# Kernel tuning notes

Hardware: AMD Instinct MI355X
Metric: run time of the kernel (lower is better)

## Reference

```python
import jax, jax.numpy as jnp
import numpy as np

FF = 256      # ff_dim
LAT = 128     # latent_dim
ACT = 8       # action_dim
VIS = 512     # vis_dim
MIN_VAR = 0.01


def _lin(x, w, b):
    return x @ w.T + b


def _mlp2(x, w1, b1, w2, b2):
    return jax.nn.relu(_lin(jax.nn.relu(_lin(x, w1, b1)), w2, b2))


def setup_inputs() -> dict:
    key = jax.random.key(0)
    ks = jax.random.split(key, 20)
    def W(k, o, i):
        return jax.random.normal(k, (o, i), jnp.float32) / np.sqrt(i).astype(np.float32)
    def Bv(o):
        return jnp.zeros((o,), jnp.float32)
    B, T = 512, 128
    return {
        'vis_feats': jax.random.normal(ks[0], (B, T, VIS), jnp.float32),
        'actions':   jax.random.normal(ks[1], (B, T - 1, ACT), jnp.float32),
        'noise':     jax.random.normal(ks[2], (T, B, LAT), jnp.float32),
        # _obs_encode
        'w_obs1': W(ks[3], FF, VIS), 'b_obs1': Bv(FF),
        'w_obs2': W(ks[4], FF, FF),  'b_obs2': Bv(FF),
        # _gru_in
        'w_gin': W(ks[5], FF, LAT + ACT), 'b_gin': Bv(FF),
        # GRU (single layer, input FF, hidden FF)
        'w_ih': W(ks[6], 3 * FF, FF), 'w_hh': W(ks[7], 3 * FF, FF),
        'b_ih': Bv(3 * FF), 'b_hh': Bv(3 * FF),
        # _prior_layers / heads
        'w_pr1': W(ks[8], FF, FF),  'b_pr1': Bv(FF),
        'w_pr2': W(ks[9], FF, FF),  'b_pr2': Bv(FF),
        'w_prm': W(ks[10], LAT, FF), 'b_prm': Bv(LAT),
        'w_prv': W(ks[11], LAT, FF), 'b_prv': Bv(LAT),
        # _post_layers / heads (input is concat(belief, obs) -> 2*FF)
        'w_po1': W(ks[12], FF, 2 * FF), 'b_po1': Bv(FF),
        'w_po2': W(ks[13], FF, FF),     'b_po2': Bv(FF),
        'w_pom': W(ks[14], LAT, FF), 'b_pom': Bv(LAT),
        'w_pov': W(ks[15], LAT, FF), 'b_pov': Bv(LAT),
    }


def _forward(vis_feats, actions, noise,
             w_obs1, b_obs1, w_obs2, b_obs2,
             w_gin, b_gin, w_ih, w_hh, b_ih, b_hh,
             w_pr1, b_pr1, w_pr2, b_pr2, w_prm, b_prm, w_prv, b_prv,
             w_po1, b_po1, w_po2, b_po2, w_pom, b_pom, w_pov, b_pov):
    # encode: obs MLP over precomputed visual features -> [B,T,FF]
    obs = _mlp2(vis_feats, w_obs1, b_obs1, w_obs2, b_obs2)
    B = obs.shape[0]

    def posterior(belief, o, eps):
        mid = _mlp2(jnp.concatenate([belief, o], -1), w_po1, b_po1, w_po2, b_po2)
        mu = _lin(mid, w_pom, b_pom)
        var = jnp.exp(_lin(mid, w_pov, b_pov)) + MIN_VAR  # diag covariance
        return mu + jnp.sqrt(var) * eps, mu, var          # rsample

    # initial posterior with zero rnn belief
    s0, _, _ = posterior(jnp.zeros((B, FF), obs.dtype), obs[:, 0], noise[0])
    h0 = jnp.zeros((B, FF), obs.dtype)

    xs = (jnp.swapaxes(actions, 0, 1),          # [T-1,B,ACT]
          jnp.swapaxes(obs[:, 1:], 0, 1),       # [T-1,B,FF]
          noise[1:])                             # [T-1,B,LAT]

    def step(carry, x):
        s, h = carry
        a, o, eps = x
        g = jax.nn.relu(_lin(jnp.concatenate([s, a], -1), w_gin, b_gin))
        # GRU cell (PyTorch gate layout: r,z,n)
        gi = _lin(g, w_ih, b_ih)
        gh = _lin(h, w_hh, b_hh)
        ir, iz, inn = jnp.split(gi, 3, -1)
        hr, hz, hn = jnp.split(gh, 3, -1)
        r = jax.nn.sigmoid(ir + hr)
        z = jax.nn.sigmoid(iz + hz)
        n = jnp.tanh(inn + r * hn)
        h_new = (1.0 - z) * n + z * h             # rnn belief
        # prior head
        pm = _mlp2(h_new, w_pr1, b_pr1, w_pr2, b_pr2)
        mu_p = _lin(pm, w_prm, b_prm)
        var_p = jnp.exp(_lin(pm, w_prv, b_prv)) + MIN_VAR
        # posterior head + reparameterized sample
        s_new, mu_q, var_q = posterior(h_new, o, eps)
        # KL(posterior || prior) for diagonal Gaussians (== MVN with diag cov)
        kl = 0.5 * jnp.sum(jnp.log(var_p) - jnp.log(var_q)
                           + (var_q + (mu_q - mu_p) ** 2) / var_p - 1.0, -1)
        return (s_new, h_new), (s_new, kl)

    _, (ss, kls) = jax.lax.scan(step, (s0, h0), xs)
    states = jnp.concatenate([s0[:, None], jnp.swapaxes(ss, 0, 1)], 1)  # [B,T,LAT]
    kl = jnp.swapaxes(kls, 0, 1)                                         # [B,T-1]
    return states, kl


def reference(vis_feats, actions, noise,
              w_obs1, b_obs1, w_obs2, b_obs2,
              w_gin, b_gin, w_ih, w_hh, b_ih, b_hh,
              w_pr1, b_pr1, w_pr2, b_pr2, w_prm, b_prm, w_prv, b_prv,
              w_po1, b_po1, w_po2, b_po2, w_pom, b_pom, w_pov, b_pov):
    return _forward(vis_feats, actions, noise,
                    w_obs1, b_obs1, w_obs2, b_obs2,
                    w_gin, b_gin, w_ih, w_hh, b_ih, b_hh,
                    w_pr1, b_pr1, w_pr2, b_pr2, w_prm, b_prm, w_prv, b_prv,
                    w_po1, b_po1, w_po2, b_po2, w_pom, b_pom, w_pov, b_pov)
```

## Files before the change

### kernel.cpp

```cpp
#include <hip/hip_runtime.h>
#include <math.h>


using v8s   = __attribute__((ext_vector_type(8))) short;
using f32x4 = __attribute__((ext_vector_type(4))) float;
typedef unsigned long long u64;

#define BN   512
#define TN   128
#define LATN 128

#define AB_S 264
#define SA_S 136

#define OBS1_T 0
#define OBS2_T 256
#define PO1O_T 384
#define PO1H_T 512
#define GINS_T 640
#define IH_T   704
#define HH_T   1088
#define PR1_T  1472
#define PR2_T  1600
#define PRM_T  1728
#define PRV_T  1792
#define PO2_T  1856
#define POM_T  1984
#define POV_T  2048
#define TOT_TILES 2112

#define B1_BYTES 33554432UL
#define KL_OFF   8388608UL

#define GIN_L 0
#define IH_L  8
#define HH_L  56
#define P1_L  104
#define P2_L  120
#define NLT   136

__device__ __forceinline__ unsigned short f2bf(float f){
  union { float f; unsigned u; } v; v.f = f;
  unsigned u = v.u + 0x7fffu + ((v.u >> 16) & 1u);
  return (unsigned short)(u >> 16);
}
__device__ __forceinline__ float bf2f(unsigned short s){
  union { unsigned u; float f; } v; v.u = ((unsigned)s) << 16; return v.f;
}
__device__ __forceinline__ float sigm(float x){ return 1.f / (1.f + __expf(-x)); }
__device__ __forceinline__ float tanhx(float x){ return 1.f - 2.f/(__expf(2.f*x) + 1.f); }

#define MFMA16(a,b,c) __builtin_amdgcn_mfma_f32_16x16x32_bf16((a),(b),(c),0,0,0)
#define LDB(tIdx) (*(const v8s*)(wt + ((size_t)(tIdx))*512 + lane*8))

__device__ __forceinline__ void stx16(unsigned short* p, v8s v){
  union { u64 u[2]; v8s v; } x; x.v = v;
  __hip_atomic_store((u64*)p,     x.u[0], __ATOMIC_RELAXED, __HIP_MEMORY_SCOPE_AGENT);
  __hip_atomic_store((u64*)p + 1, x.u[1], __ATOMIC_RELAXED, __HIP_MEMORY_SCOPE_AGENT);
}
__device__ __forceinline__ v8s ldx16(const unsigned short* p){
  union { u64 u[2]; v8s v; } x;
  x.u[0] = __hip_atomic_load((u64*)p,     __ATOMIC_RELAXED, __HIP_MEMORY_SCOPE_AGENT);
  x.u[1] = __hip_atomic_load((u64*)p + 1, __ATOMIC_RELAXED, __HIP_MEMORY_SCOPE_AGENT);
  return x.v;
}
__device__ __forceinline__ void stxs(unsigned short* p, unsigned short v){
  __hip_atomic_store(p, v, __ATOMIC_RELAXED, __HIP_MEMORY_SCOPE_AGENT);
}

struct ShufArgs {
  const float* src[14];
  int stride[14], coloff[14], ktiles[14], tbase[14], tcnt[14];
};

__global__ __launch_bounds__(64) void shuffle_w(ShufArgs sa, unsigned short* __restrict__ wt)
{
  int tile = blockIdx.x;
  int s = 0;
  while (tile >= sa.tbase[s] + sa.tcnt[s]) s++;
  int lt = tile - sa.tbase[s];
  int kt = lt % sa.ktiles[s];
  int nt = lt / sa.ktiles[s];
  int l  = threadIdx.x;
  int n  = nt*16 + (l & 15);
  int k  = sa.coloff[s] + kt*32 + (l >> 4)*8;
  const float* sp = sa.src[s] + (size_t)n * sa.stride[s] + k;
  unsigned short* dp = wt + (size_t)tile*512 + (size_t)l*8;
  #pragma unroll
  for (int j = 0; j < 8; j++) dp[j] = f2bf(sp[j]);
}

__global__ __launch_bounds__(256) void big_gemm(
    const void* __restrict__ Ain, int aIsF32, int K,
    const unsigned short* __restrict__ wt, int tbase,
    const float* __restrict__ bias, int doRelu,
    unsigned short* __restrict__ outB)
{
  __shared__ unsigned short AL[64*AB_S];
  int tid = threadIdx.x, lane = tid & 63, wv = tid >> 6;
  int q = lane >> 4, c16 = lane & 15;
  size_t row0 = (size_t)blockIdx.x * 64;

  f32x4 acc[16];
  #pragma unroll
  for (int nt = 0; nt < 16; nt++) acc[nt] = (f32x4){0.f,0.f,0.f,0.f};

  int nchunk = K >> 8;
  int ktT    = K >> 5;
  for (int cc = 0; cc < nchunk; cc++){
    int r = tid >> 2, c0 = (tid & 3) * 64;
    if (aIsF32){
      const float* A = (const float*)Ain + (row0 + r) * (size_t)K + (size_t)cc*256 + c0;
      #pragma unroll
      for (int ii = 0; ii < 16; ii++){
        float4 x = ((const float4*)A)[ii];
        ushort4 o;
        o.x = f2bf(x.x); o.y = f2bf(x.y); o.z = f2bf(x.z); o.w = f2bf(x.w);
        *(ushort4*)&AL[r*AB_S + c0 + ii*4] = o;
      }
    } else {
      const unsigned short* A = (const unsigned short*)Ain + (row0 + r)*256 + c0;
      #pragma unroll
      for (int ii = 0; ii < 8; ii++)
        *(v8s*)&AL[r*AB_S + c0 + ii*8] = *(const v8s*)(A + ii*8);
    }
    __syncthreads();
    const unsigned short* myA = &AL[wv*16*AB_S];
    #pragma unroll
    for (int kt = 0; kt < 8; kt++){
      v8s af = *(const v8s*)&myA[c16*AB_S + kt*32 + q*8];
      #pragma unroll
      for (int nt = 0; nt < 16; nt++){
        v8s bf = *(const v8s*)(wt + ((size_t)(tbase + nt*ktT + cc*8 + kt))*512 + lane*8);
        acc[nt] = MFMA16(af, bf, acc[nt]);
      }
    }
    __syncthreads();
  }
  #pragma unroll
  for (int nt = 0; nt < 16; nt++){
    int col = nt*16 + c16;
    float b = bias[col];
    #pragma unroll
    for (int i = 0; i < 4; i++){
      float v = acc[nt][i] + b;
      if (doRelu) v = fmaxf(v, 0.f);
      outB[(row0 + wv*16 + q*4 + i)*256 + col] = f2bf(v);
    }
  }
}

__device__ __forceinline__ void stage256(
    const unsigned short* __restrict__ inA,
    const unsigned short* __restrict__ wt, int tbase,
    const float* __restrict__ bias,
    unsigned short* __restrict__ outA, int lane, int wv)
{
  int q = lane >> 4, c16 = lane & 15;
  v8s wf[8];
  #pragma unroll
  for (int kt = 0; kt < 8; kt++) wf[kt] = LDB(tbase + wv*8 + kt);
  v8s af[8];
  #pragma unroll
  for (int kt = 0; kt < 8; kt++) af[kt] = *(const v8s*)&inA[c16*AB_S + kt*32 + q*8];
  f32x4 acc = (f32x4){0.f,0.f,0.f,0.f};
  #pragma unroll
  for (int kt = 0; kt < 8; kt++) acc = MFMA16(af[kt], wf[kt], acc);
  int col = wv*16 + c16;
  float b = bias[col];
  #pragma unroll
  for (int i = 0; i < 4; i++)
    outA[(q*4 + i)*AB_S + col] = f2bf(fmaxf(acc[i] + b, 0.f));
}

__device__ __forceinline__ void pheads(
    const unsigned short* __restrict__ X2,
    const unsigned short* __restrict__ wt, int tM, int tV,
    const float* __restrict__ bM, const float* __restrict__ bV,
    float* __restrict__ muF, float* __restrict__ varF, int lane, int wv)
{
  int q = lane >> 4, c16 = lane & 15;
  int mtx = wv >> 3, nt = wv & 7;
  int tb  = mtx ? tV : tM;
  v8s wf[8];
  #pragma unroll
  for (int kt = 0; kt < 8; kt++) wf[kt] = LDB(tb + nt*8 + kt);
  v8s af[8];
  #pragma unroll
  for (int kt = 0; kt < 8; kt++) af[kt] = *(const v8s*)&X2[c16*AB_S + kt*32 + q*8];
  f32x4 acc = (f32x4){0.f,0.f,0.f,0.f};
  #pragma unroll
  for (int kt = 0; kt < 8; kt++) acc = MFMA16(af[kt], wf[kt], acc);
  int col = nt*16 + c16;
  float b = mtx ? bV[col] : bM[col];
  float* dst = mtx ? varF : muF;
  #pragma unroll
  for (int i = 0; i < 4; i++){
    float v = acc[i] + b;
    if (mtx) v = __expf(v) + 0.01f;
    dst[(q*4 + i)*LATN + col] = v;
  }
}

__device__ __forceinline__ void pstage_add(
    const unsigned short* __restrict__ inA,
    const unsigned short* __restrict__ wt, int tbase,
    const unsigned short* __restrict__ Pbuf, int row0,
    unsigned short* __restrict__ outA, int lane, int wv)
{
  int q = lane >> 4, c16 = lane & 15;
  v8s wf[8];
  #pragma unroll
  for (int kt = 0; kt < 8; kt++) wf[kt] = LDB(tbase + wv*8 + kt);
  v8s af[8];
  #pragma unroll
  for (int kt = 0; kt < 8; kt++) af[kt] = *(const v8s*)&inA[c16*AB_S + kt*32 + q*8];
  int col = wv*16 + c16;
  unsigned short pv[4];
  #pragma unroll
  for (int i = 0; i < 4; i++){
    int grow = row0 + q*4 + i;
    int prow = grow + grow/127 + 1;
    pv[i] = __builtin_nontemporal_load(&Pbuf[(size_t)prow*256 + col]);
  }
  f32x4 acc = (f32x4){0.f,0.f,0.f,0.f};
  #pragma unroll
  for (int kt = 0; kt < 8; kt++) acc = MFMA16(af[kt], wf[kt], acc);
  #pragma unroll
  for (int i = 0; i < 4; i++){
    float v = acc[i] + bf2f(pv[i]);
    outA[(q*4 + i)*AB_S + col] = f2bf(fmaxf(v, 0.f));
  }
}

__device__ __forceinline__ void gsync(unsigned* c, unsigned tgt, int tid)
{
  __syncthreads();
  asm volatile("" ::: "memory");
  if (tid == 0){
    __hip_atomic_fetch_add(c, 1u, __ATOMIC_RELAXED, __HIP_MEMORY_SCOPE_AGENT);
    while (__hip_atomic_load(c, __ATOMIC_RELAXED, __HIP_MEMORY_SCOPE_AGENT) < tgt)
      __builtin_amdgcn_s_sleep(1);
  }
  asm volatile("" ::: "memory");
  __syncthreads();
}

struct RnnArgs {
  const unsigned short *wt, *Pbuf;
  const float *actions, *noise, *w_gin, *b_gin, *b_ih, *b_hh, *b_po2, *b_pom, *b_pov;
  unsigned short *Hb, *XS, *XG, *XH, *XM1, *XM2;
  unsigned *cnt;
  float *out;
};

__global__ __launch_bounds__(128, 1) void rssm_rnn(RnnArgs A)
{
  __shared__ unsigned short Lw[NLT*512];
  __shared__ float LwaA[256];
  __shared__ float Lbg[32], Lbih[96], Lbhh[96], Lbp2[32], Lbm[16], Lbv[16];
  __shared__ float muv[2][16][16];
  __shared__ float aF[128];

  int tid = threadIdx.x, lane = tid & 63, wv = tid >> 6;
  int q = lane >> 4, c16 = lane & 15;
  int g = blockIdx.x & 31, j = blockIdx.x >> 5;
  int b0 = g * 16;
  int lc = wv*16 + c16;
  int gc = 32*j + lc;

  for (int u = tid; u < NLT*64; u += 128){
    int lt = u >> 6, ch = u & 63;
    int gt;
    if (lt < 8){
      int w = lt >> 2, kt = lt & 3;
      gt = GINS_T + (2*j + w)*4 + kt;
    } else if (lt < 56){
      int u2 = lt - 8;
      gt = IH_T + ((u2 >> 4)*16 + 2*j + ((u2 >> 3) & 1))*8 + (u2 & 7);
    } else if (lt < 104){
      int u2 = lt - 56;
      gt = HH_T + ((u2 >> 4)*16 + 2*j + ((u2 >> 3) & 1))*8 + (u2 & 7);
    } else if (lt < 120){
      int u2 = lt - 104;
      gt = PO1H_T + (2*j + (u2 >> 3))*8 + (u2 & 7);
    } else {
      int u2 = lt - 120;
      gt = PO2_T + (2*j + (u2 >> 3))*8 + (u2 & 7);
    }
    *(v8s*)&Lw[lt*512 + ch*8] = *(const v8s*)(A.wt + (size_t)gt*512 + ch*8);
  }
  for (int u = tid; u < 256; u += 128)
    LwaA[u] = A.w_gin[(size_t)(32*j + (u >> 3))*136 + 128 + (u & 7)];
  if (tid < 32){ Lbg[tid] = A.b_gin[32*j + tid]; Lbp2[tid] = A.b_po2[32*j + tid]; }
  if (tid >= 32 && tid < 128){
    int u = tid - 32;
    if (u < 96){
      Lbih[u] = A.b_ih[(u >> 5)*256 + 32*j + (u & 31)];
      Lbhh[u] = A.b_hh[(u >> 5)*256 + 32*j + (u & 31)];
    }
  }
  if (tid < 16){ Lbm[tid] = A.b_pom[16*j + tid]; Lbv[tid] = A.b_pov[16*j + tid]; }

  v8s wh[8];
  {
    const unsigned short* wt = A.wt;
    int tb = (wv ? POV_T : POM_T) + j*8;
    #pragma unroll
    for (int kt = 0; kt < 8; kt++) wh[kt] = LDB(tb + kt);
  }
  float hFr[4] = {0.f, 0.f, 0.f, 0.f};
  __syncthreads();

  unsigned* cS  = A.cnt + g*16 + 0;
  unsigned* cG  = A.cnt + g*16 + 1;
  unsigned* cH  = A.cnt + g*16 + 2;
  unsigned* cM1 = A.cnt + g*16 + 3;
  unsigned* cM2 = A.cnt + g*16 + 4;
  const size_t sl = (size_t)(g*8);

  for (int t = -1; t < TN-1; t++){
    unsigned e2 = (unsigned)(8*(t+2));
    if (t >= 0){
      aF[tid] = __builtin_nontemporal_load(
          &A.actions[((size_t)(b0 + (tid >> 3))*127 + t)*8 + (tid & 7)]);
      __syncthreads();
      {
        v8s af4[4], wf[4];
        #pragma unroll
        for (int kt = 0; kt < 4; kt++)
          af4[kt] = ldx16(A.XS + ((sl + 2*kt + (q >> 1))*16 + c16)*16 + (q & 1)*8);
        #pragma unroll
        for (int kt = 0; kt < 4; kt++)
          wf[kt] = *(const v8s*)&Lw[(GIN_L + wv*4 + kt)*512 + lane*8];
        f32x4 acc = (f32x4){0.f,0.f,0.f,0.f};
        #pragma unroll
        for (int kt = 0; kt < 4; kt++) acc = MFMA16(af4[kt], wf[kt], acc);
        float bg = Lbg[lc];
        #pragma unroll
        for (int i = 0; i < 4; i++){
          int r = q*4 + i;
          float v = acc[i] + bg;
          #pragma unroll
          for (int m = 0; m < 8; m++) v += aF[r*8 + m]*LwaA[lc*8 + m];
          stxs(&A.XG[((sl + j)*16 + r)*32 + lc], f2bf(fmaxf(v, 0.f)));
        }
      }
      gsync(cG, (unsigned)(8*(t+1)), tid);
      {
        int p = t & 1;
        v8s ag[8], ah[8];
        #pragma unroll
        for (int kt = 0; kt < 8; kt++){
          ag[kt] = ldx16(A.XG + ((sl + kt)*16 + c16)*32 + q*8);
          ah[kt] = ldx16(A.XH + (((size_t)p*256 + sl + kt)*16 + c16)*32 + q*8);
        }
        f32x4 accI[3];
        #pragma unroll
        for (int x = 0; x < 3; x++){
          v8s wf[8];
          #pragma unroll
          for (int kt = 0; kt < 8; kt++)
            wf[kt] = *(const v8s*)&Lw[(IH_L + (x*2 + wv)*8 + kt)*512 + lane*8];
          accI[x] = (f32x4){0.f,0.f,0.f,0.f};
          #pragma unroll
          for (int kt = 0; kt < 8; kt++) accI[x] = MFMA16(ag[kt], wf[kt], accI[x]);
        }
        float rg[4], zg[4];
        {
          v8s wf[8];
          #pragma unroll
          for (int kt = 0; kt < 8; kt++)
            wf[kt] = *(const v8s*)&Lw[(HH_L + (0*2 + wv)*8 + kt)*512 + lane*8];
          f32x4 a = (f32x4){0.f,0.f,0.f,0.f};
          #pragma unroll
          for (int kt = 0; kt < 8; kt++) a = MFMA16(ah[kt], wf[kt], a);
          float bir = Lbih[lc], bhr = Lbhh[lc];
          #pragma unroll
          for (int i = 0; i < 4; i++) rg[i] = sigm(accI[0][i] + bir + a[i] + bhr);
        }
        {
          v8s wf[8];
          #pragma unroll
          for (int kt = 0; kt < 8; kt++)
            wf[kt] = *(const v8s*)&Lw[(HH_L + (1*2 + wv)*8 + kt)*512 + lane*8];
          f32x4 a = (f32x4){0.f,0.f,0.f,0.f};
          #pragma unroll
          for (int kt = 0; kt < 8; kt++) a = MFMA16(ah[kt], wf[kt], a);
          float biz = Lbih[32 + lc], bhz = Lbhh[32 + lc];
          #pragma unroll
          for (int i = 0; i < 4; i++) zg[i] = sigm(accI[1][i] + biz + a[i] + bhz);
        }
        {
          v8s wf[8];
          #pragma unroll
          for (int kt = 0; kt < 8; kt++)
            wf[kt] = *(const v8s*)&Lw[(HH_L + (2*2 + wv)*8 + kt)*512 + lane*8];
          f32x4 a = (f32x4){0.f,0.f,0.f,0.f};
          #pragma unroll
          for (int kt = 0; kt < 8; kt++) a = MFMA16(ah[kt], wf[kt], a);
          float bin = Lbih[64 + lc], bhn = Lbhh[64 + lc];
          #pragma unroll
          for (int i = 0; i < 4; i++){
            int r = q*4 + i;
            float ng = tanhx(accI[2][i] + bin + rg[i]*(a[i] + bhn));
            float hv = (1.f - zg[i])*ng + zg[i]*hFr[i];
            hFr[i] = hv;
            unsigned short hb = f2bf(hv);
            stxs(&A.XH[(((size_t)(1 - p)*256 + sl + j)*16 + r)*32 + lc], hb);
            __builtin_nontemporal_store(hb, &A.Hb[((size_t)(b0 + r)*127 + t)*256 + gc]);
          }
        }
      }
      gsync(cH, (unsigned)(8*(t+1)), tid);
      {
        int p = t & 1;
        v8s ah[8], wf[8];
        #pragma unroll
        for (int kt = 0; kt < 8; kt++)
          ah[kt] = ldx16(A.XH + (((size_t)(1 - p)*256 + sl + kt)*16 + c16)*32 + q*8);
        #pragma unroll
        for (int kt = 0; kt < 8; kt++)
          wf[kt] = *(const v8s*)&Lw[(P1_L + wv*8 + kt)*512 + lane*8];
        unsigned short pv[4];
        #pragma unroll
        for (int i = 0; i < 4; i++)
          pv[i] = __builtin_nontemporal_load(
              &A.Pbuf[((size_t)(b0 + q*4 + i)*TN + (t+1))*256 + gc]);
        f32x4 acc = (f32x4){0.f,0.f,0.f,0.f};
        #pragma unroll
        for (int kt = 0; kt < 8; kt++) acc = MFMA16(ah[kt], wf[kt], acc);
        #pragma unroll
        for (int i = 0; i < 4; i++)
          stxs(&A.XM1[((sl + j)*16 + q*4 + i)*32 + lc],
               f2bf(fmaxf(acc[i] + bf2f(pv[i]), 0.f)));
      }
    } else {
      #pragma unroll
      for (int i = 0; i < 4; i++){
        int r = q*4 + i;
        unsigned short pv = __builtin_nontemporal_load(
            &A.Pbuf[((size_t)(b0 + r)*TN + 0)*256 + gc]);
        stxs(&A.XM1[((sl + j)*16 + r)*32 + lc], f2bf(fmaxf(bf2f(pv), 0.f)));
      }
    }
    gsync(cM1, e2, tid);
    {
      v8s am[8], wf[8];
      #pragma unroll
      for (int kt = 0; kt < 8; kt++)
        am[kt] = ldx16(A.XM1 + ((sl + kt)*16 + c16)*32 + q*8);
      #pragma unroll
      for (int kt = 0; kt < 8; kt++)
        wf[kt] = *(const v8s*)&Lw[(P2_L + wv*8 + kt)*512 + lane*8];
      f32x4 acc = (f32x4){0.f,0.f,0.f,0.f};
      #pragma unroll
      for (int kt = 0; kt < 8; kt++) acc = MFMA16(am[kt], wf[kt], acc);
      #pragma unroll
      for (int i = 0; i < 4; i++)
        stxs(&A.XM2[((sl + j)*16 + q*4 + i)*32 + lc],
             f2bf(fmaxf(acc[i] + Lbp2[lc], 0.f)));
    }
    gsync(cM2, e2, tid);
    {
      v8s am[8];
      #pragma unroll
      for (int kt = 0; kt < 8; kt++)
        am[kt] = ldx16(A.XM2 + ((sl + kt)*16 + c16)*32 + q*8);
      f32x4 acc = (f32x4){0.f,0.f,0.f,0.f};
      #pragma unroll
      for (int kt = 0; kt < 8; kt++) acc = MFMA16(am[kt], wh[kt], acc);
      #pragma unroll
      for (int i = 0; i < 4; i++){
        float v = acc[i] + (wv ? Lbv[c16] : Lbm[c16]);
        if (wv) v = __expf(v) + 0.01f;
        muv[wv][q*4 + i][c16] = v;
      }
    }
    __syncthreads();
    for (int u = tid; u < 256; u += 128){
      int r = u >> 4, c = u & 15;
      float mq = muv[0][r][c], vq = muv[1][r][c];
      float ep = __builtin_nontemporal_load(
          &A.noise[((size_t)(t+1)*BN + b0 + r)*LATN + 16*j + c]);
      float sv = mq + sqrtf(vq)*ep;
      __builtin_nontemporal_store(sv, &A.out[((size_t)(b0 + r)*TN + (t+1))*LATN + 16*j + c]);
      stxs(&A.XS[(sl + j)*256 + r*16 + c], f2bf(sv));
    }
    gsync(cS, e2, tid);
  }
}

__global__ __launch_bounds__(1024, 4) void post_pass(
    const unsigned short* __restrict__ wt,
    const unsigned short* __restrict__ Pbuf,
    const unsigned short* __restrict__ Hb,
    const float* __restrict__ b_pr1, const float* __restrict__ b_pr2,
    const float* __restrict__ b_prm, const float* __restrict__ b_prv,
    const float* __restrict__ b_po2, const float* __restrict__ b_pom,
    const float* __restrict__ b_pov,
    float* __restrict__ out)
{
  __shared__ unsigned short hC[16*AB_S];
  __shared__ unsigned short X1[16*AB_S];
  __shared__ unsigned short X2[16*AB_S];
  __shared__ float mupF[16*LATN], varpF[16*LATN];
  __shared__ float muqF[16*LATN], varqF[16*LATN];

  int tid = threadIdx.x, lane = tid & 63, wv = tid >> 6;
  int row0 = blockIdx.x * 16;

  if (tid < 512){
    int r = tid >> 5, c8 = (tid & 31)*8;
    *(v8s*)&hC[r*AB_S + c8] = *(const v8s*)&Hb[(size_t)(row0 + r)*256 + c8];
  }
  __syncthreads();

  stage256(hC, wt, PR1_T, b_pr1, X1, lane, wv);
  __syncthreads();
  stage256(X1, wt, PR2_T, b_pr2, X2, lane, wv);
  __syncthreads();
  pheads(X2, wt, PRM_T, PRV_T, b_prm, b_prv, mupF, varpF, lane, wv);
  __syncthreads();

  pstage_add(hC, wt, PO1H_T, Pbuf, row0, X1, lane, wv);
  __syncthreads();
  stage256(X1, wt, PO2_T, b_po2, X2, lane, wv);
  __syncthreads();
  pheads(X2, wt, POM_T, POV_T, b_pom, b_pov, muqF, varqF, lane, wv);
  __syncthreads();

  {
    int r = wv;
    float kv = 0.f;
    #pragma unroll
    for (int ii = 0; ii < 2; ii++){
      int c = lane + ii*64;
      float mq = muqF[r*LATN + c], vq = varqF[r*LATN + c];
      float mp = mupF[r*LATN + c], vp = varpF[r*LATN + c];
      float d = mq - mp;
      kv += __logf(vp) - __logf(vq) + (vq + d*d)/vp - 1.f;
    }
    #pragma unroll
    for (int m = 1; m < 64; m <<= 1) kv += __shfl_xor(kv, m, 64);
    if (lane == 0)
      __builtin_nontemporal_store(0.5f*kv, &out[KL_OFF + (size_t)(row0 + r)]);
  }
}

extern "C" void kernel_launch(void* const* d_in, const int* in_sizes, int n_in,
                              void* d_out, int out_size, void* d_ws, size_t ws_size,
                              hipStream_t stream)
{
  (void)in_sizes; (void)n_in; (void)out_size; (void)ws_size;
  const float* vis    = (const float*)d_in[0];
  const float* acts   = (const float*)d_in[1];
  const float* noise  = (const float*)d_in[2];
  const float* w_obs1 = (const float*)d_in[3];
  const float* b_obs1 = (const float*)d_in[4];
  const float* w_obs2 = (const float*)d_in[5];
  const float* b_obs2 = (const float*)d_in[6];
  const float* w_gin  = (const float*)d_in[7];
  const float* b_gin  = (const float*)d_in[8];
  const float* w_ih   = (const float*)d_in[9];
  const float* w_hh   = (const float*)d_in[10];
  const float* b_ih   = (const float*)d_in[11];
  const float* b_hh   = (const float*)d_in[12];
  const float* w_pr1  = (const float*)d_in[13];
  const float* b_pr1  = (const float*)d_in[14];
  const float* w_pr2  = (const float*)d_in[15];
  const float* b_pr2  = (const float*)d_in[16];
  const float* w_prm  = (const float*)d_in[17];
  const float* b_prm  = (const float*)d_in[18];
  const float* w_prv  = (const float*)d_in[19];
  const float* b_prv  = (const float*)d_in[20];
  const float* w_po1  = (const float*)d_in[21];
  const float* b_po1  = (const float*)d_in[22];
  const float* w_po2  = (const float*)d_in[23];
  const float* b_po2  = (const float*)d_in[24];
  const float* w_pom  = (const float*)d_in[25];
  const float* b_pom  = (const float*)d_in[26];
  const float* w_pov  = (const float*)d_in[27];
  const float* b_pov  = (const float*)d_in[28];

  unsigned short* B1 = (unsigned short*)d_ws;
  unsigned short* WT = (unsigned short*)((char*)d_ws + B1_BYTES);
  unsigned short* Hb  = WT + (size_t)TOT_TILES*512;
  unsigned short* XS  = Hb + (size_t)BN*127*256;
  unsigned short* XG  = XS + 32*8*256;
  unsigned short* XH  = XG + 32*8*512;
  unsigned short* XM1 = XH + (size_t)2*32*8*512;
  unsigned short* XM2 = XM1 + 32*8*512;
  unsigned*       CNT = (unsigned*)(XM2 + 32*8*512);

  ShufArgs sa;
  const float* srcs[14] = {w_obs1, w_obs2, w_po1, w_po1, w_gin, w_ih, w_hh,
                           w_pr1, w_pr2, w_prm, w_prv, w_po2, w_pom, w_pov};
  const int strides[14] = {512,256,512,512,136,256,256,256,256,256,256,256,256,256};
  const int coloffs[14] = {0,0,256,0,0,0,0,0,0,0,0,0,0,0};
  const int ktl[14]     = {16,8,8,8,4,8,8,8,8,8,8,8,8,8};
  const int tbas[14]    = {OBS1_T,OBS2_T,PO1O_T,PO1H_T,GINS_T,IH_T,HH_T,
                           PR1_T,PR2_T,PRM_T,PRV_T,PO2_T,POM_T,POV_T};
  const int tcnt[14]    = {256,128,128,128,64,384,384,128,128,64,64,128,64,64};
  for (int i = 0; i < 14; i++){
    sa.src[i] = srcs[i]; sa.stride[i] = strides[i]; sa.coloff[i] = coloffs[i];
    sa.ktiles[i] = ktl[i]; sa.tbase[i] = tbas[i]; sa.tcnt[i] = tcnt[i];
  }
  shuffle_w<<<TOT_TILES, 64, 0, stream>>>(sa, WT);

  big_gemm<<<1024, 256, 0, stream>>>(vis, 1, 512, WT, OBS1_T, b_obs1, 1, B1);
  big_gemm<<<1024, 256, 0, stream>>>(B1,  0, 256, WT, OBS2_T, b_obs2, 1, B1);
  big_gemm<<<1024, 256, 0, stream>>>(B1,  0, 256, WT, PO1O_T, b_po1,  0, B1);

  hipMemsetAsync(XH, 0, (size_t)2*32*8*512*2, stream);
  hipMemsetAsync(CNT, 0, 32*16*4, stream);

  RnnArgs ra;
  ra.wt = WT; ra.Pbuf = B1;
  ra.actions = acts; ra.noise = noise; ra.w_gin = w_gin;
  ra.b_gin = b_gin; ra.b_ih = b_ih; ra.b_hh = b_hh;
  ra.b_po2 = b_po2; ra.b_pom = b_pom; ra.b_pov = b_pov;
  ra.Hb = Hb; ra.XS = XS; ra.XG = XG; ra.XH = XH; ra.XM1 = XM1; ra.XM2 = XM2;
  ra.cnt = CNT; ra.out = (float*)d_out;
  rssm_rnn<<<256, 128, 0, stream>>>(ra);

  post_pass<<<4064, 1024, 0, stream>>>(WT, B1, Hb, b_pr1, b_pr2, b_prm, b_prv,
                                       b_po2, b_pom, b_pov, (float*)d_out);
}
```

Measured before the change: 2.064 ms.

## Replace counter barriers with per-block epoch flags and compute posterior heads redundantly

The recurrent kernel's group barrier changes from a shared atomic counter to per-block epoch flags that eight threads poll in parallel. Each block now computes the full mu/var posterior heads for its 16 rows locally, which removes the sample-exchange buffer (XS) and one grid barrier per step. XH, Pbuf and action loads are also issued before the barriers to overlap with the waits. The post-pass processes four 16-row sub-tiles per block with a quarter as many blocks. The cost is 8x redundant head computation, with head weights now read from global memory each step instead of held in registers.

```diff
diff --git a/kernel.cpp b/kernel.cpp
--- a/kernel.cpp
+++ b/kernel.cpp
@@ -11,7 +11,6 @@
 #define LATN 128
 
 #define AB_S 264
-#define SA_S 136
 
 #define OBS1_T 0
 #define OBS2_T 256
@@ -53,11 +52,6 @@
 #define MFMA16(a,b,c) __builtin_amdgcn_mfma_f32_16x16x32_bf16((a),(b),(c),0,0,0)
 #define LDB(tIdx) (*(const v8s*)(wt + ((size_t)(tIdx))*512 + lane*8))
 
-__device__ __forceinline__ void stx16(unsigned short* p, v8s v){
-  union { u64 u[2]; v8s v; } x; x.v = v;
-  __hip_atomic_store((u64*)p,     x.u[0], __ATOMIC_RELAXED, __HIP_MEMORY_SCOPE_AGENT);
-  __hip_atomic_store((u64*)p + 1, x.u[1], __ATOMIC_RELAXED, __HIP_MEMORY_SCOPE_AGENT);
-}
 __device__ __forceinline__ v8s ldx16(const unsigned short* p){
   union { u64 u[2]; v8s v; } x;
   x.u[0] = __hip_atomic_load((u64*)p,     __ATOMIC_RELAXED, __HIP_MEMORY_SCOPE_AGENT);
@@ -233,24 +227,23 @@
   }
 }
 
-__device__ __forceinline__ void gsync(unsigned* c, unsigned tgt, int tid)
+__device__ __forceinline__ void gsync(unsigned* f8, int j, unsigned ep, int tid)
 {
   __syncthreads();
-  asm volatile("" ::: "memory");
-  if (tid == 0){
-    __hip_atomic_fetch_add(c, 1u, __ATOMIC_RELAXED, __HIP_MEMORY_SCOPE_AGENT);
-    while (__hip_atomic_load(c, __ATOMIC_RELAXED, __HIP_MEMORY_SCOPE_AGENT) < tgt)
+  if (tid == 0)
+    __hip_atomic_store(f8 + j, ep, __ATOMIC_RELAXED, __HIP_MEMORY_SCOPE_AGENT);
+  if (tid < 8){
+    while (__hip_atomic_load(f8 + tid, __ATOMIC_RELAXED, __HIP_MEMORY_SCOPE_AGENT) < ep)
       __builtin_amdgcn_s_sleep(1);
   }
-  asm volatile("" ::: "memory");
   __syncthreads();
 }
 
 struct RnnArgs {
   const unsigned short *wt, *Pbuf;
   const float *actions, *noise, *w_gin, *b_gin, *b_ih, *b_hh, *b_po2, *b_pom, *b_pov;
-  unsigned short *Hb, *XS, *XG, *XH, *XM1, *XM2;
-  unsigned *cnt;
+  unsigned short *Hb, *XG, *XH, *XM1, *XM2;
+  unsigned *flg;
   float *out;
 };
 
@@ -258,8 +251,10 @@
 {
   __shared__ unsigned short Lw[NLT*512];
   __shared__ float LwaA[256];
-  __shared__ float Lbg[32], Lbih[96], Lbhh[96], Lbp2[32], Lbm[16], Lbv[16];
-  __shared__ float muv[2][16][16];
+  __shared__ float Lbg[32], Lbih[96], Lbhh[96], Lbp2[32];
+  __shared__ float Lbm[128], Lbv[128];
+  __shared__ float varF[16*128];
+  __shared__ unsigned short sF[16*136];
   __shared__ float aF[128];
 
   int tid = threadIdx.x, lane = tid & 63, wv = tid >> 6;
@@ -300,36 +295,26 @@
       Lbhh[u] = A.b_hh[(u >> 5)*256 + 32*j + (u & 31)];
     }
   }
-  if (tid < 16){ Lbm[tid] = A.b_pom[16*j + tid]; Lbv[tid] = A.b_pov[16*j + tid]; }
-
-  v8s wh[8];
-  {
-    const unsigned short* wt = A.wt;
-    int tb = (wv ? POV_T : POM_T) + j*8;
-    #pragma unroll
-    for (int kt = 0; kt < 8; kt++) wh[kt] = LDB(tb + kt);
-  }
+  Lbm[tid] = A.b_pom[tid];
+  Lbv[tid] = A.b_pov[tid];
+
   float hFr[4] = {0.f, 0.f, 0.f, 0.f};
   __syncthreads();
 
-  unsigned* cS  = A.cnt + g*16 + 0;
-  unsigned* cG  = A.cnt + g*16 + 1;
-  unsigned* cH  = A.cnt + g*16 + 2;
-  unsigned* cM1 = A.cnt + g*16 + 3;
-  unsigned* cM2 = A.cnt + g*16 + 4;
+  unsigned* FG  = A.flg + (0*32 + g)*8;
+  unsigned* FH  = A.flg + (1*32 + g)*8;
+  unsigned* FM1 = A.flg + (2*32 + g)*8;
+  unsigned* FM2 = A.flg + (3*32 + g)*8;
   const size_t sl = (size_t)(g*8);
 
   for (int t = -1; t < TN-1; t++){
-    unsigned e2 = (unsigned)(8*(t+2));
     if (t >= 0){
-      aF[tid] = __builtin_nontemporal_load(
-          &A.actions[((size_t)(b0 + (tid >> 3))*127 + t)*8 + (tid & 7)]);
-      __syncthreads();
+      int p = t & 1;
       {
         v8s af4[4], wf[4];
         #pragma unroll
         for (int kt = 0; kt < 4; kt++)
-          af4[kt] = ldx16(A.XS + ((sl + 2*kt + (q >> 1))*16 + c16)*16 + (q & 1)*8);
+          af4[kt] = *(const v8s*)&sF[c16*136 + kt*32 + q*8];
         #pragma unroll
         for (int kt = 0; kt < 4; kt++)
           wf[kt] = *(const v8s*)&Lw[(GIN_L + wv*4 + kt)*512 + lane*8];
@@ -346,15 +331,16 @@
           stxs(&A.XG[((sl + j)*16 + r)*32 + lc], f2bf(fmaxf(v, 0.f)));
         }
       }
-      gsync(cG, (unsigned)(8*(t+1)), tid);
+      v8s ah[8];
+      #pragma unroll
+      for (int kt = 0; kt < 8; kt++)
+        ah[kt] = ldx16(A.XH + (((size_t)p*256 + sl + kt)*16 + c16)*32 + q*8);
+      gsync(FG, j, (unsigned)(t+1), tid);
       {
-        int p = t & 1;
-        v8s ag[8], ah[8];
-        #pragma unroll
-        for (int kt = 0; kt < 8; kt++){
+        v8s ag[8];
+        #pragma unroll
+        for (int kt = 0; kt < 8; kt++)
           ag[kt] = ldx16(A.XG + ((sl + kt)*16 + c16)*32 + q*8);
-          ah[kt] = ldx16(A.XH + (((size_t)p*256 + sl + kt)*16 + c16)*32 + q*8);
-        }
         f32x4 accI[3];
         #pragma unroll
         for (int x = 0; x < 3; x++){
@@ -412,24 +398,23 @@
           }
         }
       }
-      gsync(cH, (unsigned)(8*(t+1)), tid);
+      unsigned short pv[4];
+      #pragma unroll
+      for (int i = 0; i < 4; i++)
+        pv[i] = __builtin_nontemporal_load(
+            &A.Pbuf[((size_t)(b0 + q*4 + i)*TN + (t+1))*256 + gc]);
+      gsync(FH, j, (unsigned)(t+1), tid);
       {
-        int p = t & 1;
-        v8s ah[8], wf[8];
+        v8s ah2[8], wf[8];
         #pragma unroll
         for (int kt = 0; kt < 8; kt++)
-          ah[kt] = ldx16(A.XH + (((size_t)(1 - p)*256 + sl + kt)*16 + c16)*32 + q*8);
+          ah2[kt] = ldx16(A.XH + (((size_t)(1 - p)*256 + sl + kt)*16 + c16)*32 + q*8);
         #pragma unroll
         for (int kt = 0; kt < 8; kt++)
           wf[kt] = *(const v8s*)&Lw[(P1_L + wv*8 + kt)*512 + lane*8];
-        unsigned short pv[4];
-        #pragma unroll
-        for (int i = 0; i < 4; i++)
-          pv[i] = __builtin_nontemporal_load(
-              &A.Pbuf[((size_t)(b0 + q*4 + i)*TN + (t+1))*256 + gc]);
         f32x4 acc = (f32x4){0.f,0.f,0.f,0.f};
         #pragma unroll
-        for (int kt = 0; kt < 8; kt++) acc = MFMA16(ah[kt], wf[kt], acc);
+        for (int kt = 0; kt < 8; kt++) acc = MFMA16(ah2[kt], wf[kt], acc);
         #pragma unroll
         for (int i = 0; i < 4; i++)
           stxs(&A.XM1[((sl + j)*16 + q*4 + i)*32 + lc],
@@ -439,12 +424,12 @@
       #pragma unroll
       for (int i = 0; i < 4; i++){
         int r = q*4 + i;
-        unsigned short pv = __builtin_nontemporal_load(
+        unsigned short pv0 = __builtin_nontemporal_load(
             &A.Pbuf[((size_t)(b0 + r)*TN + 0)*256 + gc]);
-        stxs(&A.XM1[((sl + j)*16 + r)*32 + lc], f2bf(fmaxf(bf2f(pv), 0.f)));
-      }
-    }
-    gsync(cM1, e2, tid);
+        stxs(&A.XM1[((sl + j)*16 + r)*32 + lc], f2bf(fmaxf(bf2f(pv0), 0.f)));
+      }
+    }
+    gsync(FM1, j, (unsigned)(t+2), tid);
     {
       v8s am[8], wf[8];
       #pragma unroll
@@ -461,33 +446,54 @@
         stxs(&A.XM2[((sl + j)*16 + q*4 + i)*32 + lc],
              f2bf(fmaxf(acc[i] + Lbp2[lc], 0.f)));
     }
-    gsync(cM2, e2, tid);
+    gsync(FM2, j, (unsigned)(t+2), tid);
     {
       v8s am[8];
       #pragma unroll
       for (int kt = 0; kt < 8; kt++)
         am[kt] = ldx16(A.XM2 + ((sl + kt)*16 + c16)*32 + q*8);
-      f32x4 acc = (f32x4){0.f,0.f,0.f,0.f};
-      #pragma unroll
-      for (int kt = 0; kt < 8; kt++) acc = MFMA16(am[kt], wh[kt], acc);
-      #pragma unroll
-      for (int i = 0; i < 4; i++){
-        float v = acc[i] + (wv ? Lbv[c16] : Lbm[c16]);
-        if (wv) v = __expf(v) + 0.01f;
-        muv[wv][q*4 + i][c16] = v;
-      }
-    }
-    __syncthreads();
-    for (int u = tid; u < 256; u += 128){
-      int r = u >> 4, c = u & 15;
-      float mq = muv[0][r][c], vq = muv[1][r][c];
-      float ep = __builtin_nontemporal_load(
-          &A.noise[((size_t)(t+1)*BN + b0 + r)*LATN + 16*j + c]);
-      float sv = mq + sqrtf(vq)*ep;
-      __builtin_nontemporal_store(sv, &A.out[((size_t)(b0 + r)*TN + (t+1))*LATN + 16*j + c]);
-      stxs(&A.XS[(sl + j)*256 + r*16 + c], f2bf(sv));
-    }
-    gsync(cS, e2, tid);
+      const unsigned short* wt = A.wt;
+      int tb = wv ? POV_T : POM_T;
+      f32x4 acc2[8];
+      #pragma unroll
+      for (int nt = 0; nt < 8; nt++){
+        acc2[nt] = (f32x4){0.f,0.f,0.f,0.f};
+        #pragma unroll
+        for (int kt = 0; kt < 8; kt++)
+          acc2[nt] = MFMA16(am[kt], LDB(tb + nt*8 + kt), acc2[nt]);
+      }
+      if (wv){
+        #pragma unroll
+        for (int nt = 0; nt < 8; nt++)
+          #pragma unroll
+          for (int i = 0; i < 4; i++)
+            varF[(q*4 + i)*128 + nt*16 + c16] =
+                __expf(acc2[nt][i] + Lbv[nt*16 + c16]) + 0.01f;
+      }
+      if (t + 1 < TN - 1)
+        aF[tid] = __builtin_nontemporal_load(
+            &A.actions[((size_t)(b0 + (tid >> 3))*127 + (t+1))*8 + (tid & 7)]);
+      __syncthreads();
+      if (!wv){
+        #pragma unroll
+        for (int nt = 0; nt < 8; nt++){
+          #pragma unroll
+          for (int i = 0; i < 4; i++){
+            int r = q*4 + i, c = nt*16 + c16;
+            float mq = acc2[nt][i] + Lbm[c];
+            float vq = varF[r*128 + c];
+            float ep2 = __builtin_nontemporal_load(
+                &A.noise[((size_t)(t+1)*BN + b0 + r)*LATN + c]);
+            float sv = mq + sqrtf(vq)*ep2;
+            sF[r*136 + c] = f2bf(sv);
+            if (nt == j)
+              __builtin_nontemporal_store(sv,
+                  &A.out[((size_t)(b0 + r)*TN + (t+1))*LATN + c]);
+          }
+        }
+      }
+      __syncthreads();
+    }
   }
 }
 
@@ -508,43 +514,47 @@
   __shared__ float muqF[16*LATN], varqF[16*LATN];
 
   int tid = threadIdx.x, lane = tid & 63, wv = tid >> 6;
-  int row0 = blockIdx.x * 16;
-
-  if (tid < 512){
-    int r = tid >> 5, c8 = (tid & 31)*8;
-    *(v8s*)&hC[r*AB_S + c8] = *(const v8s*)&Hb[(size_t)(row0 + r)*256 + c8];
-  }
-  __syncthreads();
-
-  stage256(hC, wt, PR1_T, b_pr1, X1, lane, wv);
-  __syncthreads();
-  stage256(X1, wt, PR2_T, b_pr2, X2, lane, wv);
-  __syncthreads();
-  pheads(X2, wt, PRM_T, PRV_T, b_prm, b_prv, mupF, varpF, lane, wv);
-  __syncthreads();
-
-  pstage_add(hC, wt, PO1H_T, Pbuf, row0, X1, lane, wv);
-  __syncthreads();
-  stage256(X1, wt, PO2_T, b_po2, X2, lane, wv);
-  __syncthreads();
-  pheads(X2, wt, POM_T, POV_T, b_pom, b_pov, muqF, varqF, lane, wv);
-  __syncthreads();
-
-  {
-    int r = wv;
-    float kv = 0.f;
-    #pragma unroll
-    for (int ii = 0; ii < 2; ii++){
-      int c = lane + ii*64;
-      float mq = muqF[r*LATN + c], vq = varqF[r*LATN + c];
-      float mp = mupF[r*LATN + c], vp = varpF[r*LATN + c];
-      float d = mq - mp;
-      kv += __logf(vp) - __logf(vq) + (vq + d*d)/vp - 1.f;
-    }
-    #pragma unroll
-    for (int m = 1; m < 64; m <<= 1) kv += __shfl_xor(kv, m, 64);
-    if (lane == 0)
-      __builtin_nontemporal_store(0.5f*kv, &out[KL_OFF + (size_t)(row0 + r)]);
+
+  for (int sub = 0; sub < 4; sub++){
+    int row0 = blockIdx.x * 64 + sub * 16;
+
+    if (tid < 512){
+      int r = tid >> 5, c8 = (tid & 31)*8;
+      *(v8s*)&hC[r*AB_S + c8] = *(const v8s*)&Hb[(size_t)(row0 + r)*256 + c8];
+    }
+    __syncthreads();
+
+    stage256(hC, wt, PR1_T, b_pr1, X1, lane, wv);
+    __syncthreads();
+    stage256(X1, wt, PR2_T, b_pr2, X2, lane, wv);
+    __syncthreads();
+    pheads(X2, wt, PRM_T, PRV_T, b_prm, b_prv, mupF, varpF, lane, wv);
+    __syncthreads();
+
+    pstage_add(hC, wt, PO1H_T, Pbuf, row0, X1, lane, wv);
+    __syncthreads();
+    stage256(X1, wt, PO2_T, b_po2, X2, lane, wv);
+    __syncthreads();
+    pheads(X2, wt, POM_T, POV_T, b_pom, b_pov, muqF, varqF, lane, wv);
+    __syncthreads();
+
+    {
+      int r = wv;
+      float kv = 0.f;
+      #pragma unroll
+      for (int ii = 0; ii < 2; ii++){
+        int c = lane + ii*64;
+        float mq = muqF[r*LATN + c], vq = varqF[r*LATN + c];
+        float mp = mupF[r*LATN + c], vp = varpF[r*LATN + c];
+        float d = mq - mp;
+        kv += __logf(vp) - __logf(vq) + (vq + d*d)/vp - 1.f;
+      }
+      #pragma unroll
+      for (int m = 1; m < 64; m <<= 1) kv += __shfl_xor(kv, m, 64);
+      if (lane == 0)
+        __builtin_nontemporal_store(0.5f*kv, &out[KL_OFF + (size_t)(row0 + r)]);
+    }
+    __syncthreads();
   }
 }
 
@@ -586,12 +596,11 @@
   unsigned short* B1 = (unsigned short*)d_ws;
   unsigned short* WT = (unsigned short*)((char*)d_ws + B1_BYTES);
   unsigned short* Hb  = WT + (size_t)TOT_TILES*512;
-  unsigned short* XS  = Hb + (size_t)BN*127*256;
-  unsigned short* XG  = XS + 32*8*256;
+  unsigned short* XG  = Hb + (size_t)BN*127*256;
   unsigned short* XH  = XG + 32*8*512;
   unsigned short* XM1 = XH + (size_t)2*32*8*512;
   unsigned short* XM2 = XM1 + 32*8*512;
-  unsigned*       CNT = (unsigned*)(XM2 + 32*8*512);
+  unsigned*       FLG = (unsigned*)(XM2 + 32*8*512);
 
   ShufArgs sa;
   const float* srcs[14] = {w_obs1, w_obs2, w_po1, w_po1, w_gin, w_ih, w_hh,
@@ -613,17 +622,17 @@
   big_gemm<<<1024, 256, 0, stream>>>(B1,  0, 256, WT, PO1O_T, b_po1,  0, B1);
 
   hipMemsetAsync(XH, 0, (size_t)2*32*8*512*2, stream);
-  hipMemsetAsync(CNT, 0, 32*16*4, stream);
+  hipMemsetAsync(FLG, 0, 4*32*8*4, stream);
 
   RnnArgs ra;
   ra.wt = WT; ra.Pbuf = B1;
   ra.actions = acts; ra.noise = noise; ra.w_gin = w_gin;
   ra.b_gin = b_gin; ra.b_ih = b_ih; ra.b_hh = b_hh;
   ra.b_po2 = b_po2; ra.b_pom = b_pom; ra.b_pov = b_pov;
-  ra.Hb = Hb; ra.XS = XS; ra.XG = XG; ra.XH = XH; ra.XM1 = XM1; ra.XM2 = XM2;
-  ra.cnt = CNT; ra.out = (float*)d_out;
+  ra.Hb = Hb; ra.XG = XG; ra.XH = XH; ra.XM1 = XM1; ra.XM2 = XM2;
+  ra.flg = FLG; ra.out = (float*)d_out;
   rssm_rnn<<<256, 128, 0, stream>>>(ra);
 
-  post_pass<<<4064, 1024, 0, stream>>>(WT, B1, Hb, b_pr1, b_pr2, b_prm, b_prv,
+  post_pass<<<1016, 1024, 0, stream>>>(WT, B1, Hb, b_pr1, b_pr2, b_prm, b_prv,
                                        b_po2, b_pom, b_pov, (float*)d_out);
 }
```

Result: slower. 3.784 ms (+83.3%).

## Use XCC-local cheaper sync and exchange when a block group shares one XCD

Applied to the files above, without the earlier changes.

Each block of the recurrent kernel records its XCC id. If all 8 blocks of a batch group sit on the same XCC, the group switches to workgroup-scope atomics and plain volatile loads and stores for counters and exchange buffers, so traffic stays in the shared L2 instead of going through agent-scope coherence. It also moves the Pbuf loads ahead of a group barrier to hide their latency. Correctness depends on the hardware-register XCC id and on volatile accesses seeing each other's writes within one XCD's L2. It adds an extra global barrier at startup. The fast path only helps when the dispatcher places a whole group on one XCD.

```diff
diff --git a/kernel.cpp b/kernel.cpp
--- a/kernel.cpp
+++ b/kernel.cpp
@@ -53,19 +53,26 @@
 #define MFMA16(a,b,c) __builtin_amdgcn_mfma_f32_16x16x32_bf16((a),(b),(c),0,0,0)
 #define LDB(tIdx) (*(const v8s*)(wt + ((size_t)(tIdx))*512 + lane*8))
 
-__device__ __forceinline__ void stx16(unsigned short* p, v8s v){
-  union { u64 u[2]; v8s v; } x; x.v = v;
-  __hip_atomic_store((u64*)p,     x.u[0], __ATOMIC_RELAXED, __HIP_MEMORY_SCOPE_AGENT);
-  __hip_atomic_store((u64*)p + 1, x.u[1], __ATOMIC_RELAXED, __HIP_MEMORY_SCOPE_AGENT);
-}
-__device__ __forceinline__ v8s ldx16(const unsigned short* p){
+__device__ __forceinline__ unsigned getXcc(){
+  unsigned x;
+  asm volatile("s_getreg_b32 %0, hwreg(20, 0, 32)" : "=s"(x));
+  return x & 0xffu;
+}
+
+__device__ __forceinline__ void stxs(unsigned short* p, unsigned short v, bool fast){
+  if (fast) *(volatile unsigned short*)p = v;
+  else      __hip_atomic_store(p, v, __ATOMIC_RELAXED, __HIP_MEMORY_SCOPE_AGENT);
+}
+__device__ __forceinline__ v8s ldx16(const unsigned short* p, bool fast){
   union { u64 u[2]; v8s v; } x;
-  x.u[0] = __hip_atomic_load((u64*)p,     __ATOMIC_RELAXED, __HIP_MEMORY_SCOPE_AGENT);
-  x.u[1] = __hip_atomic_load((u64*)p + 1, __ATOMIC_RELAXED, __HIP_MEMORY_SCOPE_AGENT);
+  if (fast){
+    x.u[0] = *(volatile const u64*)p;
+    x.u[1] = *((volatile const u64*)p + 1);
+  } else {
+    x.u[0] = __hip_atomic_load((u64*)p,     __ATOMIC_RELAXED, __HIP_MEMORY_SCOPE_AGENT);
+    x.u[1] = __hip_atomic_load((u64*)p + 1, __ATOMIC_RELAXED, __HIP_MEMORY_SCOPE_AGENT);
+  }
   return x.v;
-}
-__device__ __forceinline__ void stxs(unsigned short* p, unsigned short v){
-  __hip_atomic_store(p, v, __ATOMIC_RELAXED, __HIP_MEMORY_SCOPE_AGENT);
 }
 
 struct ShufArgs {
@@ -233,14 +240,20 @@
   }
 }
 
-__device__ __forceinline__ void gsync(unsigned* c, unsigned tgt, int tid)
+__device__ __forceinline__ void gsync(unsigned* c, unsigned tgt, int tid, bool fast)
 {
   __syncthreads();
   asm volatile("" ::: "memory");
   if (tid == 0){
-    __hip_atomic_fetch_add(c, 1u, __ATOMIC_RELAXED, __HIP_MEMORY_SCOPE_AGENT);
-    while (__hip_atomic_load(c, __ATOMIC_RELAXED, __HIP_MEMORY_SCOPE_AGENT) < tgt)
-      __builtin_amdgcn_s_sleep(1);
+    if (fast){
+      __hip_atomic_fetch_add(c, 1u, __ATOMIC_RELAXED, __HIP_MEMORY_SCOPE_WORKGROUP);
+      while (*(volatile unsigned*)c < tgt)
+        __builtin_amdgcn_s_sleep(1);
+    } else {
+      __hip_atomic_fetch_add(c, 1u, __ATOMIC_RELAXED, __HIP_MEMORY_SCOPE_AGENT);
+      while (__hip_atomic_load(c, __ATOMIC_RELAXED, __HIP_MEMORY_SCOPE_AGENT) < tgt)
+        __builtin_amdgcn_s_sleep(1);
+    }
   }
   asm volatile("" ::: "memory");
   __syncthreads();
@@ -251,6 +264,8 @@
   const float *actions, *noise, *w_gin, *b_gin, *b_ih, *b_hh, *b_po2, *b_pom, *b_pov;
   unsigned short *Hb, *XS, *XG, *XH, *XM1, *XM2;
   unsigned *cnt;
+  unsigned *fcnt;
+  unsigned *xcc;
   float *out;
 };
 
@@ -310,13 +325,30 @@
     for (int kt = 0; kt < 8; kt++) wh[kt] = LDB(tb + kt);
   }
   float hFr[4] = {0.f, 0.f, 0.f, 0.f};
-  __syncthreads();
-
-  unsigned* cS  = A.cnt + g*16 + 0;
-  unsigned* cG  = A.cnt + g*16 + 1;
-  unsigned* cH  = A.cnt + g*16 + 2;
-  unsigned* cM1 = A.cnt + g*16 + 3;
-  unsigned* cM2 = A.cnt + g*16 + 4;
+
+  if (tid == 0)
+    __hip_atomic_store(A.xcc + blockIdx.x, getXcc(),
+                       __ATOMIC_RELAXED, __HIP_MEMORY_SCOPE_AGENT);
+  gsync(A.cnt + 512 + g, 8u, tid, false);
+  bool fast;
+  {
+    unsigned x0 = __hip_atomic_load(A.xcc + g, __ATOMIC_RELAXED, __HIP_MEMORY_SCOPE_AGENT);
+    bool eq = true;
+    #pragma unroll
+    for (int u = 1; u < 8; u++)
+      eq &= (__hip_atomic_load(A.xcc + g + 32*u, __ATOMIC_RELAXED,
+                               __HIP_MEMORY_SCOPE_AGENT) == x0);
+    unsigned xn = __hip_atomic_load(A.xcc + ((g + 1) & 31), __ATOMIC_RELAXED,
+                                    __HIP_MEMORY_SCOPE_AGENT);
+    fast = eq && (xn != x0);
+  }
+  __syncthreads();
+
+  unsigned* cS  = (fast ? A.fcnt + g*64 + 0 : A.cnt + g*16 + 0);
+  unsigned* cG  = (fast ? A.fcnt + g*64 + 1 : A.cnt + g*16 + 1);
+  unsigned* cH  = (fast ? A.fcnt + g*64 + 2 : A.cnt + g*16 + 2);
+  unsigned* cM1 = (fast ? A.fcnt + g*64 + 3 : A.cnt + g*16 + 3);
+  unsigned* cM2 = (fast ? A.fcnt + g*64 + 4 : A.cnt + g*16 + 4);
   const size_t sl = (size_t)(g*8);
 
   for (int t = -1; t < TN-1; t++){
@@ -329,7 +361,7 @@
         v8s af4[4], wf[4];
         #pragma unroll
         for (int kt = 0; kt < 4; kt++)
-          af4[kt] = ldx16(A.XS + ((sl + 2*kt + (q >> 1))*16 + c16)*16 + (q & 1)*8);
+          af4[kt] = ldx16(A.XS + ((sl + 2*kt + (q >> 1))*16 + c16)*16 + (q & 1)*8, fast);
         #pragma unroll
         for (int kt = 0; kt < 4; kt++)
           wf[kt] = *(const v8s*)&Lw[(GIN_L + wv*4 + kt)*512 + lane*8];
@@ -343,17 +375,17 @@
           float v = acc[i] + bg;
           #pragma unroll
           for (int m = 0; m < 8; m++) v += aF[r*8 + m]*LwaA[lc*8 + m];
-          stxs(&A.XG[((sl + j)*16 + r)*32 + lc], f2bf(fmaxf(v, 0.f)));
+          stxs(&A.XG[((sl + j)*16 + r)*32 + lc], f2bf(fmaxf(v, 0.f)), fast);
         }
       }
-      gsync(cG, (unsigned)(8*(t+1)), tid);
+      gsync(cG, (unsigned)(8*(t+1)), tid, fast);
       {
         int p = t & 1;
         v8s ag[8], ah[8];
         #pragma unroll
         for (int kt = 0; kt < 8; kt++){
-          ag[kt] = ldx16(A.XG + ((sl + kt)*16 + c16)*32 + q*8);
-          ah[kt] = ldx16(A.XH + (((size_t)p*256 + sl + kt)*16 + c16)*32 + q*8);
+          ag[kt] = ldx16(A.XG + ((sl + kt)*16 + c16)*32 + q*8, fast);
+          ah[kt] = ldx16(A.XH + (((size_t)p*256 + sl + kt)*16 + c16)*32 + q*8, fast);
         }
         f32x4 accI[3];
         #pragma unroll
@@ -407,49 +439,49 @@
             float hv = (1.f - zg[i])*ng + zg[i]*hFr[i];
             hFr[i] = hv;
             unsigned short hb = f2bf(hv);
-            stxs(&A.XH[(((size_t)(1 - p)*256 + sl + j)*16 + r)*32 + lc], hb);
+            stxs(&A.XH[(((size_t)(1 - p)*256 + sl + j)*16 + r)*32 + lc], hb, fast);
             __builtin_nontemporal_store(hb, &A.Hb[((size_t)(b0 + r)*127 + t)*256 + gc]);
           }
         }
       }
-      gsync(cH, (unsigned)(8*(t+1)), tid);
+      unsigned short pv[4];
+      #pragma unroll
+      for (int i = 0; i < 4; i++)
+        pv[i] = __builtin_nontemporal_load(
+            &A.Pbuf[((size_t)(b0 + q*4 + i)*TN + (t+1))*256 + gc]);
+      gsync(cH, (unsigned)(8*(t+1)), tid, fast);
       {
         int p = t & 1;
-        v8s ah[8], wf[8];
+        v8s ah2[8], wf[8];
         #pragma unroll
         for (int kt = 0; kt < 8; kt++)
-          ah[kt] = ldx16(A.XH + (((size_t)(1 - p)*256 + sl + kt)*16 + c16)*32 + q*8);
+          ah2[kt] = ldx16(A.XH + (((size_t)(1 - p)*256 + sl + kt)*16 + c16)*32 + q*8, fast);
         #pragma unroll
         for (int kt = 0; kt < 8; kt++)
           wf[kt] = *(const v8s*)&Lw[(P1_L + wv*8 + kt)*512 + lane*8];
-        unsigned short pv[4];
-        #pragma unroll
-        for (int i = 0; i < 4; i++)
-          pv[i] = __builtin_nontemporal_load(
-              &A.Pbuf[((size_t)(b0 + q*4 + i)*TN + (t+1))*256 + gc]);
         f32x4 acc = (f32x4){0.f,0.f,0.f,0.f};
         #pragma unroll
-        for (int kt = 0; kt < 8; kt++) acc = MFMA16(ah[kt], wf[kt], acc);
+        for (int kt = 0; kt < 8; kt++) acc = MFMA16(ah2[kt], wf[kt], acc);
         #pragma unroll
         for (int i = 0; i < 4; i++)
           stxs(&A.XM1[((sl + j)*16 + q*4 + i)*32 + lc],
-               f2bf(fmaxf(acc[i] + bf2f(pv[i]), 0.f)));
+               f2bf(fmaxf(acc[i] + bf2f(pv[i]), 0.f)), fast);
       }
     } else {
       #pragma unroll
       for (int i = 0; i < 4; i++){
         int r = q*4 + i;
-        unsigned short pv = __builtin_nontemporal_load(
+        unsigned short pv0 = __builtin_nontemporal_load(
             &A.Pbuf[((size_t)(b0 + r)*TN + 0)*256 + gc]);
-        stxs(&A.XM1[((sl + j)*16 + r)*32 + lc], f2bf(fmaxf(bf2f(pv), 0.f)));
+        stxs(&A.XM1[((sl + j)*16 + r)*32 + lc], f2bf(fmaxf(bf2f(pv0), 0.f)), fast);
       }
     }
-    gsync(cM1, e2, tid);
+    gsync(cM1, e2, tid, fast);
     {
       v8s am[8], wf[8];
       #pragma unroll
       for (int kt = 0; kt < 8; kt++)
-        am[kt] = ldx16(A.XM1 + ((sl + kt)*16 + c16)*32 + q*8);
+        am[kt] = ldx16(A.XM1 + ((sl + kt)*16 + c16)*32 + q*8, fast);
       #pragma unroll
       for (int kt = 0; kt < 8; kt++)
         wf[kt] = *(const v8s*)&Lw[(P2_L + wv*8 + kt)*512 + lane*8];
@@ -459,14 +491,14 @@
       #pragma unroll
       for (int i = 0; i < 4; i++)
         stxs(&A.XM2[((sl + j)*16 + q*4 + i)*32 + lc],
-             f2bf(fmaxf(acc[i] + Lbp2[lc], 0.f)));
-    }
-    gsync(cM2, e2, tid);
+             f2bf(fmaxf(acc[i] + Lbp2[lc], 0.f)), fast);
+    }
+    gsync(cM2, e2, tid, fast);
     {
       v8s am[8];
       #pragma unroll
       for (int kt = 0; kt < 8; kt++)
-        am[kt] = ldx16(A.XM2 + ((sl + kt)*16 + c16)*32 + q*8);
+        am[kt] = ldx16(A.XM2 + ((sl + kt)*16 + c16)*32 + q*8, fast);
       f32x4 acc = (f32x4){0.f,0.f,0.f,0.f};
       #pragma unroll
       for (int kt = 0; kt < 8; kt++) acc = MFMA16(am[kt], wh[kt], acc);
@@ -485,9 +517,9 @@
           &A.noise[((size_t)(t+1)*BN + b0 + r)*LATN + 16*j + c]);
       float sv = mq + sqrtf(vq)*ep;
       __builtin_nontemporal_store(sv, &A.out[((size_t)(b0 + r)*TN + (t+1))*LATN + 16*j + c]);
-      stxs(&A.XS[(sl + j)*256 + r*16 + c], f2bf(sv));
-    }
-    gsync(cS, e2, tid);
+      stxs(&A.XS[(sl + j)*256 + r*16 + c], f2bf(sv), fast);
+    }
+    gsync(cS, e2, tid, fast);
   }
 }
 
@@ -592,6 +624,8 @@
   unsigned short* XM1 = XH + (size_t)2*32*8*512;
   unsigned short* XM2 = XM1 + 32*8*512;
   unsigned*       CNT = (unsigned*)(XM2 + 32*8*512);
+  unsigned*       FCNT = (unsigned*)((char*)CNT + 4096);
+  unsigned*       XCC  = (unsigned*)((char*)FCNT + 8192);
 
   ShufArgs sa;
   const float* srcs[14] = {w_obs1, w_obs2, w_po1, w_po1, w_gin, w_ih, w_hh,
@@ -613,7 +647,8 @@
   big_gemm<<<1024, 256, 0, stream>>>(B1,  0, 256, WT, PO1O_T, b_po1,  0, B1);
 
   hipMemsetAsync(XH, 0, (size_t)2*32*8*512*2, stream);
-  hipMemsetAsync(CNT, 0, 32*16*4, stream);
+  hipMemsetAsync(CNT, 0, 4096, stream);
+  hipMemsetAsync(FCNT, 0, 8192, stream);
 
   RnnArgs ra;
   ra.wt = WT; ra.Pbuf = B1;
@@ -621,7 +656,7 @@
   ra.b_gin = b_gin; ra.b_ih = b_ih; ra.b_hh = b_hh;
   ra.b_po2 = b_po2; ra.b_pom = b_pom; ra.b_pov = b_pov;
   ra.Hb = Hb; ra.XS = XS; ra.XG = XG; ra.XH = XH; ra.XM1 = XM1; ra.XM2 = XM2;
-  ra.cnt = CNT; ra.out = (float*)d_out;
+  ra.cnt = CNT; ra.fcnt = FCNT; ra.xcc = XCC; ra.out = (float*)d_out;
   rssm_rnn<<<256, 128, 0, stream>>>(ra);
 
   post_pass<<<4064, 1024, 0, stream>>>(WT, B1, Hb, b_pr1, b_pr2, b_prm, b_prv,
```

Result: slower. 4.311 ms (+108.9%).
